# Optimization experiments

Measured on AMD Instinct MI355X. Metric: run time of the kernel, lower is better.

Reference implementation:

```python
import jax, jax.numpy as jnp
import numpy as np

STDV = 0.01


def setup_inputs() -> dict:
    key = jax.random.key(0)
    ks = jax.random.split(key, 20)
    Nr, Nl, K = 1024, 1024, 32
    xn, xe, nopen, nhidden, nclose = 64, 32, 128, 64, 2
    inp = {
        'xnr': jax.random.normal(ks[0], (Nr, xn), dtype=jnp.float32),
        'xer': jax.random.normal(ks[1], (Nr, K, xe), dtype=jnp.float32),
        'ijr': jax.random.randint(ks[2], (Nr, K, 1), 0, Nr),
        'xnl': jax.random.normal(ks[3], (Nl, xn), dtype=jnp.float32),
        'xel': jax.random.normal(ks[4], (Nl, K, xe), dtype=jnp.float32),
        'ijl': jax.random.randint(ks[5], (Nl, K, 1), 0, Nl),
        # conv1 params
        'Wc1': jax.random.normal(ks[6], (nopen, xn)) * STDV,
        'Wn1': jax.random.normal(ks[7], (nopen, xn)) * STDV,
        'We1': jax.random.normal(ks[8], (nopen, xe)) * STDV,
        # conv2 params
        'Wc2': jax.random.normal(ks[9], (nopen, nopen)) * STDV,
        'Wn2': jax.random.normal(ks[10], (nopen, nopen)) * STDV,
        'We2': jax.random.normal(ks[11], (nopen, xe)) * STDV,
        # conv3 params
        'Wc3': jax.random.normal(ks[12], (nhidden, nopen)) * STDV,
        'Wn3': jax.random.normal(ks[13], (nhidden, nopen)) * STDV,
        'We3': jax.random.normal(ks[14], (nhidden, xe)) * STDV,
        # dense params
        'A1': jax.random.normal(ks[15], (2 * nhidden, nhidden)) * STDV,
        'A2': jax.random.normal(ks[16], (nhidden, 2 * nhidden)) * STDV,
        'A3': jax.random.normal(ks[17], (nclose, nhidden)) * STDV,
    }
    return inp


def _conv(x, e, ij, Wc, Wn, We):
    # x: [N, F], e: [N, K, E], ij: [N, K, 1]
    nhbrs = ij[:, :, 0]                      # [N, K]
    xnj = x[nhbrs].mean(axis=1)              # mean over K neighbors -> [N, F]
    xej = e.mean(axis=1)                     # [N, E]
    out = x @ Wc.T + xnj @ Wn.T + xej @ We.T
    return jax.nn.relu(out)


def _merge(a, b):
    # pairwise means, row-major over (i in a, j in b) -> [Na*Nb, F]
    F = a.shape[1]
    return (0.5 * (a[:, None, :] + b[None, :, :])).reshape(-1, F)


def _dense(x, A1, A2, A3):
    h = jax.nn.relu(A1 @ x.T)
    h = jax.nn.relu(A2 @ h)
    return jax.nn.relu(A3 @ h)


def reference(xnr, xer, ijr, xnl, xel, ijl,
              Wc1, Wn1, We1, Wc2, Wn2, We2, Wc3, Wn3, We3,
              A1, A2, A3):
    xl = _conv(xnl, xel, ijl, Wc1, Wn1, We1)
    xl = _conv(xl, xel, ijl, Wc2, Wn2, We2)
    xl = _conv(xl, xel, ijl, Wc3, Wn3, We3)
    xr = _conv(xnr, xer, ijr, Wc1, Wn1, We1)
    xr = _conv(xr, xer, ijr, Wc2, Wn2, We2)
    xr = _conv(xr, xer, ijr, Wc3, Wn3, We3)
    xm = _merge(xl, xr)  # forward calls merge(xnl, xnr): outer loop over ligand
    return _dense(xm, A1, A2, A3)
```

## Files before the change

kernel.cpp:

```cpp
#include <hip/hip_runtime.h>
#include <hip/hip_bf16.h>

#define NC 2048
#define NPAIR 1048576

typedef __attribute__((ext_vector_type(8))) short bf16x8;
typedef __attribute__((ext_vector_type(4))) float f32x4;
typedef __attribute__((ext_vector_type(2))) float f32x2;
typedef __attribute__((ext_vector_type(4))) unsigned int u32x4;

__device__ inline short f2bf(float f) {
    __hip_bfloat16 h = __float2bfloat16(f);
    return __builtin_bit_cast(short, h);
}
__device__ inline unsigned cvt_pk(float a, float b) {
    unsigned r;
    asm("v_cvt_pk_bf16_f32 %0, %1, %2" : "=v"(r) : "v"(a), "v"(b));
    return r;
}
__device__ inline float bfu_lo(unsigned u) { return __builtin_bit_cast(float, u << 16); }
__device__ inline float bfu_hi(unsigned u) { return __builtin_bit_cast(float, u & 0xFFFF0000u); }

template<int NIN, int K, int NOUT, bool FUSE_U, bool L1MODE>
__global__ __launch_bounds__(256) void k_layer(
        const float* __restrict__ xl, const float* __restrict__ xr,
        const int* __restrict__ ijl, const int* __restrict__ ijr,
        const float* __restrict__ el, const float* __restrict__ er,
        float* __restrict__ xejg,
        const float* __restrict__ Wc, const float* __restrict__ Wn, const float* __restrict__ We,
        const float* __restrict__ A1,
        const float* __restrict__ A2, const float* __restrict__ A3, short* __restrict__ Bpp,
        float* __restrict__ Y, short* __restrict__ UBg) {
    const int KP = K + 4;
    __shared__ float ct[4 * KP];
    __shared__ float wts[64 * 129];
    __shared__ float x3s[4 * 64];
    __shared__ float ubs[4 * 128];
    int t = threadIdx.x;
    int w = t >> 6, l = t & 63;

    if (L1MODE && blockIdx.x >= 512) {
        int base = (blockIdx.x - 512) * 1280;
#pragma unroll
        for (int k = 0; k < 5; ++k) {
            int j = base + k * 256 + t;
            if (j < 8192) {
                int ktnt = j >> 9, l2 = (j >> 3) & 63, e2 = j & 7;
                int kt = ktnt >> 2, nt = ktnt & 3;
                int m = l2 & 15;
                int o = (nt >> 1) * 32 + (m >> 2) * 8 + (nt & 1) * 4 + (m & 3);
                int kk = kt * 32 + (l2 >> 4) * 8 + e2;
                Bpp[j] = f2bf(A2[o * 128 + kk]);
            } else {
                int jj = j - 8192;
                int cp = jj >> 9, l2 = (jj >> 3) & 63, e2 = jj & 7;
                int cc = cp >> 1, p = cp & 1;
                int m = l2 & 15;
                int h2 = cc * 32 + (l2 >> 4) * 8 + e2;
                float v = (m < 2) ? A3[m * 64 + h2] : 0.f;
                short hi = f2bf(v);
                float vh = __bfloat162float(__builtin_bit_cast(__hip_bfloat16, hi));
                Bpp[j] = p ? f2bf(v - vh) : hi;
            }
        }
        return;
    }

    int c0 = blockIdx.x * 4;
    if (NIN == 128) {
#pragma unroll
        for (int p = 0; p < 2; ++p) {
            int col = p * 2 + (t >> 7), d = t & 127;
            int c = c0 + col, n = c & 1023;
            const float* xp = (c < 1024) ? xl : xr;
            ct[col * KP + d] = xp[n * NIN + d];
        }
    } else {
        int col = t >> 6, d = t & 63;
        int c = c0 + col, n = c & 1023;
        const float* xp = (c < 1024) ? xl : xr;
        ct[col * KP + d] = xp[n * NIN + d];
    }
    {
        int col = w, c = c0 + col, n = c & 1023;
        const float* xp = (c < 1024) ? xl : xr;
        const int* ijp = (c < 1024) ? ijl : ijr;
        int nb = __builtin_amdgcn_readfirstlane(n);
        if (NIN == 128) {
            int d2 = l * 2;
            float s0 = 0.f, s1 = 0.f;
#pragma unroll
            for (int k = 0; k < 32; ++k) {
                int nh = ijp[nb * 32 + k];
                f32x2 v = *(const f32x2*)&xp[nh * NIN + d2];
                s0 += v[0]; s1 += v[1];
            }
            ct[col * KP + NIN + d2]     = s0 * (1.f / 32.f);
            ct[col * KP + NIN + d2 + 1] = s1 * (1.f / 32.f);
        } else {
            float s = 0.f;
#pragma unroll
            for (int k = 0; k < 32; ++k) {
                int nh = ijp[nb * 32 + k];
                s += xp[nh * NIN + l];
            }
            ct[col * KP + NIN + l] = s * (1.f / 32.f);
        }
        if (L1MODE) {
            const float* e = ((c < 1024) ? el : er) + (c & 1023) * 1024;
            f32x4 s4 = {0.f, 0.f, 0.f, 0.f};
#pragma unroll
            for (int q = 0; q < 4; ++q) {
                f32x4 v = *(const f32x4*)(e + q * 256 + l * 4);
#pragma unroll
                for (int ee = 0; ee < 4; ++ee) s4[ee] += v[ee];
            }
#pragma unroll
            for (int m = 8; m < 64; m <<= 1) {
#pragma unroll
                for (int ee = 0; ee < 4; ++ee) s4[ee] += __shfl_xor(s4[ee], m, 64);
            }
            if (l < 8) {
#pragma unroll
                for (int ee = 0; ee < 4; ++ee) s4[ee] *= (1.f / 32.f);
                *(f32x4*)&ct[col * KP + 2 * NIN + l * 4] = s4;
                *(f32x4*)&xejg[c * 32 + l * 4] = s4;
            }
        } else {
            if (l < 32) ct[col * KP + 2 * NIN + l] = xejg[c * 32 + l];
        }
    }
    int col = w, c = c0 + col;
    float a0 = 0.f, a1 = 0.f;
    for (int d0 = 0; d0 < K; d0 += 64) {
        int cl = (K - d0 < 64) ? (K - d0) : 64;
        const float* Wsrc; int Ksrc, ds0;
        if (d0 < NIN)          { Wsrc = Wc; Ksrc = NIN; ds0 = d0; }
        else if (d0 < 2 * NIN) { Wsrc = Wn; Ksrc = NIN; ds0 = d0 - NIN; }
        else                   { Wsrc = We; Ksrc = 32;  ds0 = 0; }
        __syncthreads();
        int q4 = cl >> 2;
        for (int idx = t; idx < NOUT * q4; idx += 256) {
            int o = idx / q4, dq = idx % q4;
            f32x4 v = *(const f32x4*)&Wsrc[o * Ksrc + ds0 + dq * 4];
#pragma unroll
            for (int j = 0; j < 4; ++j)
                wts[(dq * 4 + j) * 129 + o] = v[j];
        }
        __syncthreads();
#pragma unroll 4
        for (int dd = 0; dd < cl; ++dd) {
            float xd = ct[col * KP + d0 + dd];
            a0 = fmaf(wts[dd * 129 + l], xd, a0);
            if (NOUT == 128) a1 = fmaf(wts[dd * 129 + 64 + l], xd, a1);
        }
    }
    if (NOUT == 128) {
        Y[c * 128 + l]      = fmaxf(a0, 0.f);
        Y[c * 128 + 64 + l] = fmaxf(a1, 0.f);
    } else if (!FUSE_U) {
        Y[c * 64 + l] = fmaxf(a0, 0.f);
    } else {
        x3s[col * 64 + l] = fmaxf(a0, 0.f);
        __syncthreads();
        for (int idx = t; idx < 128 * 16; idx += 256) {
            int o = idx / 16, dq = idx % 16;
            f32x4 v = *(const f32x4*)&A1[o * 64 + dq * 4];
#pragma unroll
            for (int j = 0; j < 4; ++j)
                wts[(dq * 4 + j) * 129 + o] = 0.5f * v[j];
        }
        __syncthreads();
        float u0 = 0.f, u1 = 0.f;
#pragma unroll 4
        for (int d = 0; d < 64; ++d) {
            float xd = x3s[col * 64 + d];
            u0 = fmaf(wts[d * 129 + l],      xd, u0);
            u1 = fmaf(wts[d * 129 + 64 + l], xd, u1);
        }
        Y[c * 128 + l]      = u0;
        Y[c * 128 + 64 + l] = u1;
        ubs[col * 128 + l]      = u0;
        ubs[col * 128 + 64 + l] = u1;
        __syncthreads();
        if (l < 16) {
            int j = c0 + w;
            const float* src = &ubs[w * 128 + l * 8];
            u32x4 pw;
            pw[0] = cvt_pk(src[0], src[1]);
            pw[1] = cvt_pk(src[2], src[3]);
            pw[2] = cvt_pk(src[4], src[5]);
            pw[3] = cvt_pk(src[6], src[7]);
            *(u32x4*)((char*)UBg + j * 256 + ((l * 16) ^ ((j & 7) << 4))) = pw;
        }
    }
}

__global__ __launch_bounds__(256) void k_dense(const float* __restrict__ U,
                                               const short* __restrict__ UBg,
                                               const short* __restrict__ Bpp,
                                               float* __restrict__ out) {
    __shared__ short urb[64 * 128];
    __shared__ short bpls[8192];
    int t = threadIdx.x;
    int lane = t & 63;
    int w = t >> 6;
    int j0 = blockIdx.x * 64;
    int i  = blockIdx.y * 4 + w;
    int col = lane & 15, g = lane >> 4;

    {
        const u32x4* src = (const u32x4*)((const char*)UBg + (1024 + j0) * 256);
        u32x4* dst = (u32x4*)urb;
#pragma unroll
        for (int it = 0; it < 4; ++it)
            dst[t + it * 256] = src[t + it * 256];
    }
#pragma unroll
    for (int it = 0; it < 4; ++it) {
        int idx = t + it * 256;
        *(u32x4*)&bpls[idx * 8] = *(const u32x4*)&Bpp[idx * 8];
    }

    f32x4 ulq[4][2];
#pragma unroll
    for (int kt = 0; kt < 4; ++kt) {
        const float* p = U + i * 128 + kt * 32 + g * 8;
        ulq[kt][0] = *(const f32x4*)p;
        ulq[kt][1] = *(const f32x4*)(p + 4);
    }
    bf16x8 a3f[2][2];
#pragma unroll
    for (int c = 0; c < 2; ++c)
#pragma unroll
        for (int p = 0; p < 2; ++p)
            a3f[c][p] = *(const bf16x8*)&Bpp[8192 + ((c * 2 + p) * 64 + lane) * 8];

    __syncthreads();

    const f32x4 z4 = {0.f, 0.f, 0.f, 0.f};
    const int xr = (col & 7) << 4;
    for (int jg = 0; jg < 4; ++jg) {
        unsigned bofs = 0;
        asm volatile("" : "+v"(bofs));
        int rbase = (jg * 16 + col) * 256;
        bf16x8 h1f[4];
#pragma unroll
        for (int kt = 0; kt < 4; ++kt) {
            u32x4 uw = *(const u32x4*)((const char*)urb + rbase + (((kt * 64) | (g * 16)) ^ xr));
            f32x4 ur0 = {bfu_lo(uw[0]), bfu_hi(uw[0]), bfu_lo(uw[1]), bfu_hi(uw[1])};
            f32x4 ur1 = {bfu_lo(uw[2]), bfu_hi(uw[2]), bfu_lo(uw[3]), bfu_hi(uw[3])};
            f32x4 s0 = __builtin_elementwise_max(ulq[kt][0] + ur0, z4);
            f32x4 s1 = __builtin_elementwise_max(ulq[kt][1] + ur1, z4);
            u32x4 pw;
            pw[0] = cvt_pk(s0[0], s0[1]);
            pw[1] = cvt_pk(s0[2], s0[3]);
            pw[2] = cvt_pk(s1[0], s1[1]);
            pw[3] = cvt_pk(s1[2], s1[3]);
            h1f[kt] = __builtin_bit_cast(bf16x8, pw);
        }
        f32x4 acc1[4] = {{0,0,0,0},{0,0,0,0},{0,0,0,0},{0,0,0,0}};
#pragma unroll
        for (int nt = 0; nt < 4; ++nt)
#pragma unroll
            for (int kt = 0; kt < 4; ++kt) {
                bf16x8 a2 = *(const bf16x8*)&bpls[bofs + ((kt * 4 + nt) * 64 + lane) * 8];
                acc1[nt] = __builtin_amdgcn_mfma_f32_16x16x32_bf16(a2, h1f[kt], acc1[nt], 0, 0, 0);
            }

        f32x4 accO = {0, 0, 0, 0};
#pragma unroll
        for (int c = 0; c < 2; ++c) {
            f32x4 r0 = __builtin_elementwise_max(acc1[2 * c],     z4);
            f32x4 r1 = __builtin_elementwise_max(acc1[2 * c + 1], z4);
            u32x4 pw;
            pw[0] = cvt_pk(r0[0], r0[1]);
            pw[1] = cvt_pk(r0[2], r0[3]);
            pw[2] = cvt_pk(r1[0], r1[1]);
            pw[3] = cvt_pk(r1[2], r1[3]);
            bf16x8 hb = __builtin_bit_cast(bf16x8, pw);
            accO = __builtin_amdgcn_mfma_f32_16x16x32_bf16(a3f[c][0], hb, accO, 0, 0, 0);
            accO = __builtin_amdgcn_mfma_f32_16x16x32_bf16(a3f[c][1], hb, accO, 0, 0, 0);
        }
        if (lane < 16) {
            int p = i * 1024 + j0 + jg * 16 + col;
            out[p]         = fmaxf(accO[0], 0.f);
            out[NPAIR + p] = fmaxf(accO[1], 0.f);
        }
    }
}

extern "C" void kernel_launch(void* const* d_in, const int* in_sizes, int n_in,
                              void* d_out, int out_size, void* d_ws, size_t ws_size,
                              hipStream_t stream) {
    const float* xnr = (const float*)d_in[0];
    const float* xer = (const float*)d_in[1];
    const int*   ijr = (const int*)  d_in[2];
    const float* xnl = (const float*)d_in[3];
    const float* xel = (const float*)d_in[4];
    const int*   ijl = (const int*)  d_in[5];
    const float* Wc1 = (const float*)d_in[6];
    const float* Wn1 = (const float*)d_in[7];
    const float* We1 = (const float*)d_in[8];
    const float* Wc2 = (const float*)d_in[9];
    const float* Wn2 = (const float*)d_in[10];
    const float* We2 = (const float*)d_in[11];
    const float* Wc3 = (const float*)d_in[12];
    const float* Wn3 = (const float*)d_in[13];
    const float* We3 = (const float*)d_in[14];
    const float* A1  = (const float*)d_in[15];
    const float* A2  = (const float*)d_in[16];
    const float* A3  = (const float*)d_in[17];
    float* out = (float*)d_out;

    float* ws  = (float*)d_ws;
    float* xej = ws;
    short* Bpp = (short*)(xej + 65536);
    float* XA  = xej + 65536 + 5120;
    float* XB  = XA + 262144;
    float* U   = XB + 262144;
    short* UB  = (short*)(U + 262144);

    k_layer<64, 160, 128, false, true><<<520, 256, 0, stream>>>(
        xnl, xnr, ijl, ijr, xel, xer, xej, Wc1, Wn1, We1, nullptr, A2, A3, Bpp, XA, nullptr);
    k_layer<128, 288, 128, false, false><<<512, 256, 0, stream>>>(
        XA, XA + 1024 * 128, ijl, ijr, nullptr, nullptr, xej, Wc2, Wn2, We2, nullptr,
        nullptr, nullptr, nullptr, XB, nullptr);
    k_layer<128, 288, 64, true, false><<<512, 256, 0, stream>>>(
        XB, XB + 1024 * 128, ijl, ijr, nullptr, nullptr, xej, Wc3, Wn3, We3, A1,
        nullptr, nullptr, nullptr, U, UB);
    k_dense<<<dim3(16, 256), 256, 0, stream>>>(U, UB, Bpp, out);
}
```

Measured before the change: 76.26 us.

## Fuse three conv layer kernels into one cooperative kernel with grid barriers

The three separate layer launches become a single cooperative kernel of 512 blocks that runs the three conv layers in sequence. Between layers it synchronises the whole grid with an atomic counter barrier, reset by a memset before each launch. The Bpp weight packing moves into the first 8 blocks before layer 1. This removes two kernel launch gaps, at the cost of spin-wait barriers and a required co-residency of all 512 blocks.

After: 140.8 us. 1.85x slower.

```diff
diff --git a/kernel.cpp b/kernel.cpp
--- a/kernel.cpp
+++ b/kernel.cpp
@@ -21,26 +21,174 @@
 __device__ inline float bfu_lo(unsigned u) { return __builtin_bit_cast(float, u << 16); }
 __device__ inline float bfu_hi(unsigned u) { return __builtin_bit_cast(float, u & 0xFFFF0000u); }
 
+__device__ inline void gbar(unsigned* cnt, unsigned target) {
+    __syncthreads();
+    if (threadIdx.x == 0) {
+        __hip_atomic_fetch_add(cnt, 1u, __ATOMIC_ACQ_REL, __HIP_MEMORY_SCOPE_AGENT);
+        while (__hip_atomic_load(cnt, __ATOMIC_ACQUIRE, __HIP_MEMORY_SCOPE_AGENT) < target)
+            __builtin_amdgcn_s_sleep(2);
+    }
+    __syncthreads();
+}
+
 template<int NIN, int K, int NOUT, bool FUSE_U, bool L1MODE>
-__global__ __launch_bounds__(256) void k_layer(
+__device__ void layer_body(int bid, int t,
         const float* __restrict__ xl, const float* __restrict__ xr,
         const int* __restrict__ ijl, const int* __restrict__ ijr,
         const float* __restrict__ el, const float* __restrict__ er,
         float* __restrict__ xejg,
         const float* __restrict__ Wc, const float* __restrict__ Wn, const float* __restrict__ We,
         const float* __restrict__ A1,
-        const float* __restrict__ A2, const float* __restrict__ A3, short* __restrict__ Bpp,
-        float* __restrict__ Y, short* __restrict__ UBg) {
+        float* __restrict__ Y, short* __restrict__ UBg,
+        float* ct, float* wts, float* x3s, float* ubs) {
     const int KP = K + 4;
-    __shared__ float ct[4 * KP];
+    int w = t >> 6, l = t & 63;
+    int c0 = bid * 4;
+    if (NIN == 128) {
+#pragma unroll
+        for (int p = 0; p < 2; ++p) {
+            int col = p * 2 + (t >> 7), d = t & 127;
+            int c = c0 + col, n = c & 1023;
+            const float* xp = (c < 1024) ? xl : xr;
+            ct[col * KP + d] = xp[n * NIN + d];
+        }
+    } else {
+        int col = t >> 6, d = t & 63;
+        int c = c0 + col, n = c & 1023;
+        const float* xp = (c < 1024) ? xl : xr;
+        ct[col * KP + d] = xp[n * NIN + d];
+    }
+    {
+        int col = w, c = c0 + col, n = c & 1023;
+        const float* xp = (c < 1024) ? xl : xr;
+        const int* ijp = (c < 1024) ? ijl : ijr;
+        int nb = __builtin_amdgcn_readfirstlane(n);
+        if (NIN == 128) {
+            int d2 = l * 2;
+            float s0 = 0.f, s1 = 0.f;
+#pragma unroll
+            for (int k = 0; k < 32; ++k) {
+                int nh = ijp[nb * 32 + k];
+                f32x2 v = *(const f32x2*)&xp[nh * NIN + d2];
+                s0 += v[0]; s1 += v[1];
+            }
+            ct[col * KP + NIN + d2]     = s0 * (1.f / 32.f);
+            ct[col * KP + NIN + d2 + 1] = s1 * (1.f / 32.f);
+        } else {
+            float s = 0.f;
+#pragma unroll
+            for (int k = 0; k < 32; ++k) {
+                int nh = ijp[nb * 32 + k];
+                s += xp[nh * NIN + l];
+            }
+            ct[col * KP + NIN + l] = s * (1.f / 32.f);
+        }
+        if (L1MODE) {
+            const float* e = ((c < 1024) ? el : er) + (c & 1023) * 1024;
+            f32x4 s4 = {0.f, 0.f, 0.f, 0.f};
+#pragma unroll
+            for (int q = 0; q < 4; ++q) {
+                f32x4 v = *(const f32x4*)(e + q * 256 + l * 4);
+#pragma unroll
+                for (int ee = 0; ee < 4; ++ee) s4[ee] += v[ee];
+            }
+#pragma unroll
+            for (int m = 8; m < 64; m <<= 1) {
+#pragma unroll
+                for (int ee = 0; ee < 4; ++ee) s4[ee] += __shfl_xor(s4[ee], m, 64);
+            }
+            if (l < 8) {
+#pragma unroll
+                for (int ee = 0; ee < 4; ++ee) s4[ee] *= (1.f / 32.f);
+                *(f32x4*)&ct[col * KP + 2 * NIN + l * 4] = s4;
+                *(f32x4*)&xejg[c * 32 + l * 4] = s4;
+            }
+        } else {
+            if (l < 32) ct[col * KP + 2 * NIN + l] = xejg[c * 32 + l];
+        }
+    }
+    int col = w, c = c0 + col;
+    float a0 = 0.f, a1 = 0.f;
+    for (int d0 = 0; d0 < K; d0 += 64) {
+        int cl = (K - d0 < 64) ? (K - d0) : 64;
+        const float* Wsrc; int Ksrc, ds0;
+        if (d0 < NIN)          { Wsrc = Wc; Ksrc = NIN; ds0 = d0; }
+        else if (d0 < 2 * NIN) { Wsrc = Wn; Ksrc = NIN; ds0 = d0 - NIN; }
+        else                   { Wsrc = We; Ksrc = 32;  ds0 = 0; }
+        __syncthreads();
+        int q4 = cl >> 2;
+        for (int idx = t; idx < NOUT * q4; idx += 256) {
+            int o = idx / q4, dq = idx % q4;
+            f32x4 v = *(const f32x4*)&Wsrc[o * Ksrc + ds0 + dq * 4];
+#pragma unroll
+            for (int j = 0; j < 4; ++j)
+                wts[(dq * 4 + j) * 129 + o] = v[j];
+        }
+        __syncthreads();
+#pragma unroll 4
+        for (int dd = 0; dd < cl; ++dd) {
+            float xd = ct[col * KP + d0 + dd];
+            a0 = fmaf(wts[dd * 129 + l], xd, a0);
+            if (NOUT == 128) a1 = fmaf(wts[dd * 129 + 64 + l], xd, a1);
+        }
+    }
+    if (NOUT == 128) {
+        Y[c * 128 + l]      = fmaxf(a0, 0.f);
+        Y[c * 128 + 64 + l] = fmaxf(a1, 0.f);
+    } else if (!FUSE_U) {
+        Y[c * 64 + l] = fmaxf(a0, 0.f);
+    } else {
+        x3s[col * 64 + l] = fmaxf(a0, 0.f);
+        __syncthreads();
+        for (int idx = t; idx < 128 * 16; idx += 256) {
+            int o = idx / 16, dq = idx % 16;
+            f32x4 v = *(const f32x4*)&A1[o * 64 + dq * 4];
+#pragma unroll
+            for (int j = 0; j < 4; ++j)
+                wts[(dq * 4 + j) * 129 + o] = 0.5f * v[j];
+        }
+        __syncthreads();
+        float u0 = 0.f, u1 = 0.f;
+#pragma unroll 4
+        for (int d = 0; d < 64; ++d) {
+            float xd = x3s[col * 64 + d];
+            u0 = fmaf(wts[d * 129 + l],      xd, u0);
+            u1 = fmaf(wts[d * 129 + 64 + l], xd, u1);
+        }
+        Y[c * 128 + l]      = u0;
+        Y[c * 128 + 64 + l] = u1;
+        ubs[col * 128 + l]      = u0;
+        ubs[col * 128 + 64 + l] = u1;
+        __syncthreads();
+        if (l < 16) {
+            int j = c0 + w;
+            const float* src = &ubs[w * 128 + l * 8];
+            u32x4 pw;
+            pw[0] = cvt_pk(src[0], src[1]);
+            pw[1] = cvt_pk(src[2], src[3]);
+            pw[2] = cvt_pk(src[4], src[5]);
+            pw[3] = cvt_pk(src[6], src[7]);
+            *(u32x4*)((char*)UBg + j * 256 + ((l * 16) ^ ((j & 7) << 4))) = pw;
+        }
+    }
+}
+
+__global__ void __launch_bounds__(256)
+k_conv(const float* xnl, const float* xnr, const int* ijl, const int* ijr,
+       const float* xel, const float* xer, float* xej,
+       const float* Wc1, const float* Wn1, const float* We1,
+       const float* Wc2, const float* Wn2, const float* We2,
+       const float* Wc3, const float* Wn3, const float* We3,
+       const float* A1, const float* A2, const float* A3, short* Bpp,
+       float* XA, float* XB, float* U, short* UB, unsigned* bar) {
+    __shared__ float ct[4 * 292];
     __shared__ float wts[64 * 129];
     __shared__ float x3s[4 * 64];
     __shared__ float ubs[4 * 128];
-    int t = threadIdx.x;
-    int w = t >> 6, l = t & 63;
-
-    if (L1MODE && blockIdx.x >= 512) {
-        int base = (blockIdx.x - 512) * 1280;
+    int bid = blockIdx.x, t = threadIdx.x;
+
+    if (bid < 8) {
+        int base = bid * 1280;
 #pragma unroll
         for (int k = 0; k < 5; ++k) {
             int j = base + k * 256 + t;
@@ -63,137 +211,21 @@
                 Bpp[j] = p ? f2bf(v - vh) : hi;
             }
         }
-        return;
-    }
-
-    int c0 = blockIdx.x * 4;
-    if (NIN == 128) {
-#pragma unroll
-        for (int p = 0; p < 2; ++p) {
-            int col = p * 2 + (t >> 7), d = t & 127;
-            int c = c0 + col, n = c & 1023;
-            const float* xp = (c < 1024) ? xl : xr;
-            ct[col * KP + d] = xp[n * NIN + d];
-        }
-    } else {
-        int col = t >> 6, d = t & 63;
-        int c = c0 + col, n = c & 1023;
-        const float* xp = (c < 1024) ? xl : xr;
-        ct[col * KP + d] = xp[n * NIN + d];
-    }
-    {
-        int col = w, c = c0 + col, n = c & 1023;
-        const float* xp = (c < 1024) ? xl : xr;
-        const int* ijp = (c < 1024) ? ijl : ijr;
-        int nb = __builtin_amdgcn_readfirstlane(n);
-        if (NIN == 128) {
-            int d2 = l * 2;
-            float s0 = 0.f, s1 = 0.f;
-#pragma unroll
-            for (int k = 0; k < 32; ++k) {
-                int nh = ijp[nb * 32 + k];
-                f32x2 v = *(const f32x2*)&xp[nh * NIN + d2];
-                s0 += v[0]; s1 += v[1];
-            }
-            ct[col * KP + NIN + d2]     = s0 * (1.f / 32.f);
-            ct[col * KP + NIN + d2 + 1] = s1 * (1.f / 32.f);
-        } else {
-            float s = 0.f;
-#pragma unroll
-            for (int k = 0; k < 32; ++k) {
-                int nh = ijp[nb * 32 + k];
-                s += xp[nh * NIN + l];
-            }
-            ct[col * KP + NIN + l] = s * (1.f / 32.f);
-        }
-        if (L1MODE) {
-            const float* e = ((c < 1024) ? el : er) + (c & 1023) * 1024;
-            f32x4 s4 = {0.f, 0.f, 0.f, 0.f};
-#pragma unroll
-            for (int q = 0; q < 4; ++q) {
-                f32x4 v = *(const f32x4*)(e + q * 256 + l * 4);
-#pragma unroll
-                for (int ee = 0; ee < 4; ++ee) s4[ee] += v[ee];
-            }
-#pragma unroll
-            for (int m = 8; m < 64; m <<= 1) {
-#pragma unroll
-                for (int ee = 0; ee < 4; ++ee) s4[ee] += __shfl_xor(s4[ee], m, 64);
-            }
-            if (l < 8) {
-#pragma unroll
-                for (int ee = 0; ee < 4; ++ee) s4[ee] *= (1.f / 32.f);
-                *(f32x4*)&ct[col * KP + 2 * NIN + l * 4] = s4;
-                *(f32x4*)&xejg[c * 32 + l * 4] = s4;
-            }
-        } else {
-            if (l < 32) ct[col * KP + 2 * NIN + l] = xejg[c * 32 + l];
-        }
-    }
-    int col = w, c = c0 + col;
-    float a0 = 0.f, a1 = 0.f;
-    for (int d0 = 0; d0 < K; d0 += 64) {
-        int cl = (K - d0 < 64) ? (K - d0) : 64;
-        const float* Wsrc; int Ksrc, ds0;
-        if (d0 < NIN)          { Wsrc = Wc; Ksrc = NIN; ds0 = d0; }
-        else if (d0 < 2 * NIN) { Wsrc = Wn; Ksrc = NIN; ds0 = d0 - NIN; }
-        else                   { Wsrc = We; Ksrc = 32;  ds0 = 0; }
-        __syncthreads();
-        int q4 = cl >> 2;
-        for (int idx = t; idx < NOUT * q4; idx += 256) {
-            int o = idx / q4, dq = idx % q4;
-            f32x4 v = *(const f32x4*)&Wsrc[o * Ksrc + ds0 + dq * 4];
-#pragma unroll
-            for (int j = 0; j < 4; ++j)
-                wts[(dq * 4 + j) * 129 + o] = v[j];
-        }
-        __syncthreads();
-#pragma unroll 4
-        for (int dd = 0; dd < cl; ++dd) {
-            float xd = ct[col * KP + d0 + dd];
-            a0 = fmaf(wts[dd * 129 + l], xd, a0);
-            if (NOUT == 128) a1 = fmaf(wts[dd * 129 + 64 + l], xd, a1);
-        }
-    }
-    if (NOUT == 128) {
-        Y[c * 128 + l]      = fmaxf(a0, 0.f);
-        Y[c * 128 + 64 + l] = fmaxf(a1, 0.f);
-    } else if (!FUSE_U) {
-        Y[c * 64 + l] = fmaxf(a0, 0.f);
-    } else {
-        x3s[col * 64 + l] = fmaxf(a0, 0.f);
-        __syncthreads();
-        for (int idx = t; idx < 128 * 16; idx += 256) {
-            int o = idx / 16, dq = idx % 16;
-            f32x4 v = *(const f32x4*)&A1[o * 64 + dq * 4];
-#pragma unroll
-            for (int j = 0; j < 4; ++j)
-                wts[(dq * 4 + j) * 129 + o] = 0.5f * v[j];
-        }
-        __syncthreads();
-        float u0 = 0.f, u1 = 0.f;
-#pragma unroll 4
-        for (int d = 0; d < 64; ++d) {
-            float xd = x3s[col * 64 + d];
-            u0 = fmaf(wts[d * 129 + l],      xd, u0);
-            u1 = fmaf(wts[d * 129 + 64 + l], xd, u1);
-        }
-        Y[c * 128 + l]      = u0;
-        Y[c * 128 + 64 + l] = u1;
-        ubs[col * 128 + l]      = u0;
-        ubs[col * 128 + 64 + l] = u1;
-        __syncthreads();
-        if (l < 16) {
-            int j = c0 + w;
-            const float* src = &ubs[w * 128 + l * 8];
-            u32x4 pw;
-            pw[0] = cvt_pk(src[0], src[1]);
-            pw[1] = cvt_pk(src[2], src[3]);
-            pw[2] = cvt_pk(src[4], src[5]);
-            pw[3] = cvt_pk(src[6], src[7]);
-            *(u32x4*)((char*)UBg + j * 256 + ((l * 16) ^ ((j & 7) << 4))) = pw;
-        }
-    }
+    }
+
+    layer_body<64, 160, 128, false, true>(bid, t, xnl, xnr, ijl, ijr, xel, xer, xej,
+                                          Wc1, Wn1, We1, nullptr, XA, nullptr,
+                                          ct, wts, x3s, ubs);
+    gbar(bar + 0, 512);
+    layer_body<128, 288, 128, false, false>(bid, t, XA, XA + 1024 * 128, ijl, ijr,
+                                            nullptr, nullptr, xej,
+                                            Wc2, Wn2, We2, nullptr, XB, nullptr,
+                                            ct, wts, x3s, ubs);
+    gbar(bar + 1, 512);
+    layer_body<128, 288, 64, true, false>(bid, t, XB, XB + 1024 * 128, ijl, ijr,
+                                          nullptr, nullptr, xej,
+                                          Wc3, Wn3, We3, A1, U, UB,
+                                          ct, wts, x3s, ubs);
 }
 
 __global__ __launch_bounds__(256) void k_dense(const float* __restrict__ U,
@@ -320,14 +352,19 @@
     float* XB  = XA + 262144;
     float* U   = XB + 262144;
     short* UB  = (short*)(U + 262144);
-
-    k_layer<64, 160, 128, false, true><<<520, 256, 0, stream>>>(
-        xnl, xnr, ijl, ijr, xel, xer, xej, Wc1, Wn1, We1, nullptr, A2, A3, Bpp, XA, nullptr);
-    k_layer<128, 288, 128, false, false><<<512, 256, 0, stream>>>(
-        XA, XA + 1024 * 128, ijl, ijr, nullptr, nullptr, xej, Wc2, Wn2, We2, nullptr,
-        nullptr, nullptr, nullptr, XB, nullptr);
-    k_layer<128, 288, 64, true, false><<<512, 256, 0, stream>>>(
-        XB, XB + 1024 * 128, ijl, ijr, nullptr, nullptr, xej, Wc3, Wn3, We3, A1,
-        nullptr, nullptr, nullptr, U, UB);
+    unsigned* bar = (unsigned*)(U + 262144 + 131072);
+
+    hipMemsetAsync(bar, 0, 2 * sizeof(unsigned), stream);
+
+    void* args[] = {
+        (void*)&xnl, (void*)&xnr, (void*)&ijl, (void*)&ijr,
+        (void*)&xel, (void*)&xer, (void*)&xej,
+        (void*)&Wc1, (void*)&Wn1, (void*)&We1,
+        (void*)&Wc2, (void*)&Wn2, (void*)&We2,
+        (void*)&Wc3, (void*)&Wn3, (void*)&We3,
+        (void*)&A1,  (void*)&A2,  (void*)&A3,  (void*)&Bpp,
+        (void*)&XA,  (void*)&XB,  (void*)&U,   (void*)&UB, (void*)&bar
+    };
+    hipLaunchCooperativeKernel((void*)k_conv, dim3(512), dim3(256), args, 0, stream);
     k_dense<<<dim3(16, 256), 256, 0, stream>>>(U, UB, Bpp, out);
 }
```

## Prefetch weight chunks into registers and store weights row-major for vector LDS reads

Applied to the files above, without the earlier changes.

The per-layer conv kernel now loads the next 64-column weight chunk into registers while the current chunk is being consumed. The first chunk's load is issued before the neighbor-gather phase, so global latency overlaps with the gather. Weights are stored output-major with a padded stride of 68 instead of transposed with stride 129, so each lane reads contiguous float4 vectors from LDS in the inner dot product, and the A1 staging is vectorized the same way. The register prefetch buffer (8 float4 per thread) raises register pressure and may reduce occupancy.

Measured after the change: 65.42 us. 14.2% less time.

```diff
diff --git a/kernel.cpp b/kernel.cpp
--- a/kernel.cpp
+++ b/kernel.cpp
@@ -32,8 +32,9 @@
         const float* __restrict__ A2, const float* __restrict__ A3, short* __restrict__ Bpp,
         float* __restrict__ Y, short* __restrict__ UBg) {
     const int KP = K + 4;
+    const int NCH = (K + 63) / 64;
     __shared__ float ct[4 * KP];
-    __shared__ float wts[64 * 129];
+    __shared__ float wts[128 * 68];
     __shared__ float x3s[4 * 64];
     __shared__ float ubs[4 * 128];
     int t = threadIdx.x;
@@ -67,6 +68,44 @@
     }
 
     int c0 = blockIdx.x * 4;
+
+    auto chunk_src = [&](int c5, int& Ksrc, int& ds0, int& cl) -> const float* {
+        int d0 = c5 * 64;
+        cl = (K - d0 < 64) ? (K - d0) : 64;
+        if (d0 < NIN)            { Ksrc = NIN; ds0 = d0;       return Wc; }
+        else if (d0 < 2 * NIN)   { Ksrc = NIN; ds0 = d0 - NIN; return Wn; }
+        else                     { Ksrc = 32;  ds0 = 0;        return We; }
+    };
+    f32x4 pf[8];
+    auto prefetch = [&](int c5) {
+        int Ksrc, ds0, cl;
+        const float* Wsrc = chunk_src(c5, Ksrc, ds0, cl);
+        int nel = cl * NOUT;
+#pragma unroll
+        for (int k = 0; k < 8; ++k) {
+            int idx = t * 4 + k * 1024;
+            if (idx < nel) {
+                int o = idx / cl, dd = idx % cl;
+                pf[k] = *(const f32x4*)&Wsrc[o * Ksrc + ds0 + dd];
+            }
+        }
+    };
+    auto commit = [&](int c5) {
+        int Ksrc, ds0, cl;
+        chunk_src(c5, Ksrc, ds0, cl);
+        int nel = cl * NOUT;
+#pragma unroll
+        for (int k = 0; k < 8; ++k) {
+            int idx = t * 4 + k * 1024;
+            if (idx < nel) {
+                int o = idx / cl, dd = idx % cl;
+                *(f32x4*)&wts[o * 68 + dd] = pf[k];
+            }
+        }
+    };
+
+    prefetch(0);
+
     if (NIN == 128) {
 #pragma unroll
         for (int p = 0; p < 2; ++p) {
@@ -130,29 +169,33 @@
             if (l < 32) ct[col * KP + 2 * NIN + l] = xejg[c * 32 + l];
         }
     }
+
     int col = w, c = c0 + col;
     float a0 = 0.f, a1 = 0.f;
-    for (int d0 = 0; d0 < K; d0 += 64) {
+#pragma unroll
+    for (int c5 = 0; c5 < NCH; ++c5) {
+        __syncthreads();
+        commit(c5);
+        if (c5 + 1 < NCH) prefetch(c5 + 1);
+        __syncthreads();
+        int d0 = c5 * 64;
         int cl = (K - d0 < 64) ? (K - d0) : 64;
-        const float* Wsrc; int Ksrc, ds0;
-        if (d0 < NIN)          { Wsrc = Wc; Ksrc = NIN; ds0 = d0; }
-        else if (d0 < 2 * NIN) { Wsrc = Wn; Ksrc = NIN; ds0 = d0 - NIN; }
-        else                   { Wsrc = We; Ksrc = 32;  ds0 = 0; }
-        __syncthreads();
-        int q4 = cl >> 2;
-        for (int idx = t; idx < NOUT * q4; idx += 256) {
-            int o = idx / q4, dq = idx % q4;
-            f32x4 v = *(const f32x4*)&Wsrc[o * Ksrc + ds0 + dq * 4];
-#pragma unroll
-            for (int j = 0; j < 4; ++j)
-                wts[(dq * 4 + j) * 129 + o] = v[j];
-        }
-        __syncthreads();
 #pragma unroll 4
-        for (int dd = 0; dd < cl; ++dd) {
-            float xd = ct[col * KP + d0 + dd];
-            a0 = fmaf(wts[dd * 129 + l], xd, a0);
-            if (NOUT == 128) a1 = fmaf(wts[dd * 129 + 64 + l], xd, a1);
+        for (int dd = 0; dd < cl; dd += 4) {
+            f32x4 cq = *(const f32x4*)&ct[col * KP + d0 + dd];
+            f32x4 w0 = *(const f32x4*)&wts[l * 68 + dd];
+            if (NOUT == 128) {
+                f32x4 w1 = *(const f32x4*)&wts[(64 + l) * 68 + dd];
+#pragma unroll
+                for (int j = 0; j < 4; ++j) {
+                    a0 = fmaf(w0[j], cq[j], a0);
+                    a1 = fmaf(w1[j], cq[j], a1);
+                }
+            } else {
+#pragma unroll
+                for (int j = 0; j < 4; ++j)
+                    a0 = fmaf(w0[j], cq[j], a0);
+            }
         }
     }
     if (NOUT == 128) {
@@ -163,20 +206,25 @@
     } else {
         x3s[col * 64 + l] = fmaxf(a0, 0.f);
         __syncthreads();
-        for (int idx = t; idx < 128 * 16; idx += 256) {
-            int o = idx / 16, dq = idx % 16;
-            f32x4 v = *(const f32x4*)&A1[o * 64 + dq * 4];
-#pragma unroll
-            for (int j = 0; j < 4; ++j)
-                wts[(dq * 4 + j) * 129 + o] = 0.5f * v[j];
+        for (int idx = t * 4; idx < 128 * 64; idx += 1024) {
+            int o = idx >> 6, dd = idx & 63;
+            f32x4 v = *(const f32x4*)&A1[o * 64 + dd];
+#pragma unroll
+            for (int j = 0; j < 4; ++j) v[j] *= 0.5f;
+            *(f32x4*)&wts[o * 68 + dd] = v;
         }
         __syncthreads();
         float u0 = 0.f, u1 = 0.f;
 #pragma unroll 4
-        for (int d = 0; d < 64; ++d) {
-            float xd = x3s[col * 64 + d];
-            u0 = fmaf(wts[d * 129 + l],      xd, u0);
-            u1 = fmaf(wts[d * 129 + 64 + l], xd, u1);
+        for (int d = 0; d < 64; d += 4) {
+            f32x4 cq = *(const f32x4*)&x3s[col * 64 + d];
+            f32x4 w0 = *(const f32x4*)&wts[l * 68 + d];
+            f32x4 w1 = *(const f32x4*)&wts[(64 + l) * 68 + d];
+#pragma unroll
+            for (int j = 0; j < 4; ++j) {
+                u0 = fmaf(w0[j], cq[j], u0);
+                u1 = fmaf(w1[j], cq[j], u1);
+            }
         }
         Y[c * 128 + l]      = u0;
         Y[c * 128 + 64 + l] = u1;
```
